# Performance work log

Measured on AMD Instinct MI355X. Metric: run time of the kernel, lower is better.

The kernel has to match this reference:

```python
import jax, jax.numpy as jnp
import numpy as np

N = 50000      # nodes
E = 800000     # edges
F = 64         # in_channels == out_channels
ED = 16        # edge_dim
G = 64         # graphs in batch
L = 2          # numLayers
BN_EPS = 1e-5
STD_EPS = 1e-5
AGG_DIM = F * 4 * 3  # 4 aggregators x 3 scalers


def setup_inputs() -> dict:
    key = jax.random.key(0)
    ks = jax.random.split(key, 12)
    r = lambda k, shp, fan: (jax.random.normal(k, shp, jnp.float32) / np.sqrt(fan)).astype(jnp.float32)
    return dict(
        x=jax.random.normal(ks[0], (N, F), jnp.float32),
        edge_attr=jax.random.normal(ks[1], (E, ED), jnp.float32),
        We=r(ks[2], (L, ED, F), ED), be=jnp.zeros((L, F), jnp.float32),
        Wpre=r(ks[3], (L, 3 * F, F), 3 * F), bpre=jnp.zeros((L, F), jnp.float32),
        Wpost=r(ks[4], (L, F + AGG_DIM, F), F + AGG_DIM), bpost=jnp.zeros((L, F), jnp.float32),
        Wlin=r(ks[5], (L, F, F), F), blin=jnp.zeros((L, F), jnp.float32),
        gamma=jnp.ones((L, F), jnp.float32), beta=jnp.zeros((L, F), jnp.float32),
        W1=r(ks[6], (F, 40), F), b1=jnp.zeros((40,), jnp.float32),
        W2=r(ks[7], (40, 1), 40), b2=jnp.zeros((1,), jnp.float32),
        edge_index=jax.random.randint(ks[8], (2, E), 0, N),
        batch=jnp.sort(jax.random.randint(ks[9], (N,), 0, G)),
    )


def _ceal_conv(x, src, dst, edge_attr, We, be, Wpre, bpre, Wpost, bpost, Wlin, blin, deg, amp, att):
    # PNA-style conv, towers=1, pre_layers=post_layers=1
    e = edge_attr @ We + be                                              # [E,F]
    h = jnp.concatenate([x[dst], x[src], e], axis=-1) @ Wpre + bpre      # [E,F]
    degc = jnp.maximum(deg, 1.0)[:, None]
    mean = jax.ops.segment_sum(h, dst, num_segments=N) / degc
    sq = jax.ops.segment_sum(h * h, dst, num_segments=N) / degc
    std = jnp.sqrt(jax.nn.relu(sq - mean * mean) + STD_EPS)
    has = (deg > 0)[:, None]
    mn = jnp.where(has, jax.ops.segment_min(h, dst, num_segments=N), 0.0)
    mx = jnp.where(has, jax.ops.segment_max(h, dst, num_segments=N), 0.0)
    aggs = jnp.concatenate([mean, mn, mx, std], axis=-1)                 # [N,4F]
    scaled = jnp.concatenate([aggs, aggs * amp[:, None], aggs * att[:, None]], axis=-1)  # [N,12F]
    out = jnp.concatenate([x, scaled], axis=-1) @ Wpost + bpost          # [N,F]
    return out @ Wlin + blin


def _bn(x, gamma, beta):
    mu = x.mean(0)
    var = x.var(0)  # biased, as torch BatchNorm training-mode normalization
    return (x - mu) * jax.lax.rsqrt(var + BN_EPS) * gamma + beta


def reference(x, edge_attr, We, be, Wpre, bpre, Wpost, bpost, Wlin, blin,
              gamma, beta, W1, b1, W2, b2, edge_index, batch):
    src, dst = edge_index[0], edge_index[1]
    deg = jax.ops.segment_sum(jnp.ones((E,), jnp.float32), dst, num_segments=N)
    avg_log = jnp.mean(jnp.log(deg + 1.0))
    logd = jnp.log(jnp.maximum(deg, 1.0) + 1.0)
    amp = logd / avg_log
    att = avg_log / logd
    for l in range(L):
        x = _ceal_conv(x, src, dst, edge_attr, We[l], be[l], Wpre[l], bpre[l],
                       Wpost[l], bpost[l], Wlin[l], blin[l], deg, amp, att)
        x = jax.nn.relu(_bn(x, gamma[l], beta[l]))
    cnt = jnp.maximum(jax.ops.segment_sum(jnp.ones((N,), jnp.float32), batch, num_segments=G), 1.0)
    gm = jax.ops.segment_sum(x, batch, num_segments=G) / cnt[:, None]    # global_mean_pool [G,F]
    return jax.nn.relu(gm @ W1 + b1) @ W2 + b2                           # [G,1]
```

## Files before the change

### kernel.cpp

```cpp
#include <hip/hip_runtime.h>
#include <math.h>
#include <float.h>

#define NN 50000
#define EE 800000
#define FF 64
#define EDIM 16
#define GG 64
#define NB64 782

typedef short bf16x8 __attribute__((ext_vector_type(8)));
typedef float f32x4 __attribute__((ext_vector_type(4)));

__device__ inline unsigned short bf_rne(float v) {
  unsigned int u = __float_as_uint(v);
  unsigned int r = (u + 0x7FFFu + ((u >> 16) & 1u)) >> 16;
  return (unsigned short)r;
}
__device__ inline float bf_up(unsigned short h) {
  return __uint_as_float(((unsigned int)h) << 16);
}
__device__ inline void split4(float4 v, ushort4& h, ushort4& l) {
  h.x = bf_rne(v.x); h.y = bf_rne(v.y); h.z = bf_rne(v.z); h.w = bf_rne(v.w);
  l.x = bf_rne(v.x - bf_up(h.x));
  l.y = bf_rne(v.y - bf_up(h.y));
  l.z = bf_rne(v.z - bf_up(h.z));
  l.w = bf_rne(v.w - bf_up(h.w));
}
__device__ inline float blo(unsigned int u) { return __uint_as_float(u << 16); }
__device__ inline float bhi(unsigned int u) { return __uint_as_float(u & 0xFFFF0000u); }

__global__ void k_deg(const int* __restrict__ eidx, int* __restrict__ deg) {
  int e = blockIdx.x * 256 + threadIdx.x;
  if (e < EE) atomicAdd(&deg[eidx[EE + e]], 1);
}

__global__ void k_avglog(const int* __restrict__ deg, double* __restrict__ acc) {
  int n = blockIdx.x * 256 + threadIdx.x;
  float v = (n < NN) ? logf((float)deg[n] + 1.0f) : 0.0f;
  __shared__ float s[256];
  s[threadIdx.x] = v;
  __syncthreads();
  for (int o = 128; o > 0; o >>= 1) {
    if (threadIdx.x < o) s[threadIdx.x] += s[threadIdx.x + o];
    __syncthreads();
  }
  if (threadIdx.x == 0) atomicAdd(acc, (double)s[0]);
}

__global__ __launch_bounds__(1024) void k_scan(const int* __restrict__ deg, int* __restrict__ offsets) {
  __shared__ int wsum[16];
  __shared__ int s_carry;
  int t = threadIdx.x;
  int lane = t & 63;
  int wid = t >> 6;
  if (t == 0) s_carry = 0;
  __syncthreads();
  for (int base = 0; base < NN; base += 1024) {
    int idx = base + t;
    int v = (idx < NN) ? deg[idx] : 0;
    int x = v;
    #pragma unroll
    for (int o = 1; o < 64; o <<= 1) {
      int y = __shfl_up(x, o);
      if (lane >= o) x += y;
    }
    if (lane == 63) wsum[wid] = x;
    __syncthreads();
    if (wid == 0 && lane < 16) {
      int wv = wsum[lane];
      #pragma unroll
      for (int o = 1; o < 16; o <<= 1) {
        int y = __shfl_up(wv, o);
        if (lane >= o) wv += y;
      }
      wsum[lane] = wv;
    }
    __syncthreads();
    int pre = (wid > 0 ? wsum[wid - 1] : 0) + s_carry;
    if (idx < NN) offsets[idx] = pre + x - v;
    __syncthreads();
    if (t == 0) s_carry += wsum[15];
    __syncthreads();
  }
  if (threadIdx.x == 0) offsets[NN] = s_carry;
}

__global__ void k_scatter(const int* __restrict__ eidx, const int* __restrict__ offsets,
                          int* __restrict__ cursor, int* __restrict__ srcs,
                          const float* __restrict__ eattr, unsigned int* __restrict__ PermEA) {
  int e = blockIdx.x * 256 + threadIdx.x;
  if (e < EE) {
    int s = eidx[e];
    int d = eidx[EE + e];
    int pos = offsets[d] + atomicAdd(&cursor[d], 1);
    srcs[pos] = s;
    const float4* ep = (const float4*)(eattr + (size_t)e * EDIM);
    float4 q0 = ep[0], q1 = ep[1], q2 = ep[2], q3 = ep[3];
    uint4 pa, pb;
    pa.x = (unsigned)bf_rne(q0.x) | ((unsigned)bf_rne(q0.y) << 16);
    pa.y = (unsigned)bf_rne(q0.z) | ((unsigned)bf_rne(q0.w) << 16);
    pa.z = (unsigned)bf_rne(q1.x) | ((unsigned)bf_rne(q1.y) << 16);
    pa.w = (unsigned)bf_rne(q1.z) | ((unsigned)bf_rne(q1.w) << 16);
    pb.x = (unsigned)bf_rne(q2.x) | ((unsigned)bf_rne(q2.y) << 16);
    pb.y = (unsigned)bf_rne(q2.z) | ((unsigned)bf_rne(q2.w) << 16);
    pb.z = (unsigned)bf_rne(q3.x) | ((unsigned)bf_rne(q3.y) << 16);
    pb.w = (unsigned)bf_rne(q3.z) | ((unsigned)bf_rne(q3.w) << 16);
    ((uint4*)PermEA)[(size_t)pos * 2] = pa;
    ((uint4*)PermEA)[(size_t)pos * 2 + 1] = pb;
  }
}

__global__ void k_ampatt(const int* __restrict__ deg, const double* __restrict__ acc,
                         float* __restrict__ amp, float* __restrict__ att) {
  int n = blockIdx.x * 256 + threadIdx.x;
  if (n < NN) {
    float avg = (float)(acc[0] / (double)NN);
    float d = (float)deg[n];
    float logd = logf(fmaxf(d, 1.0f) + 1.0f);
    amp[n] = logd / avg;
    att[n] = avg / logd;
  }
}

__global__ __launch_bounds__(256) void k_prep2(const float* __restrict__ We, const float* __restrict__ be,
                                               const float* __restrict__ Wpre, const float* __restrict__ bpre,
                                               const float* __restrict__ Wpost, const float* __restrict__ bpost,
                                               const float* __restrict__ Wlin, const float* __restrict__ blin,
                                               float* __restrict__ Mw, float* __restrict__ bconst,
                                               unsigned short* __restrict__ WcT_h, unsigned short* __restrict__ WcT_l,
                                               unsigned short* __restrict__ WxT_h, unsigned short* __restrict__ WxT_l,
                                               float* __restrict__ bcomb) {
  int id = blockIdx.x * 256 + threadIdx.x;
  if (id < 53248) {
    int k = id >> 6, f = id & 63;
    float a = 0.0f;
    for (int j = 0; j < FF; j++) a += Wpost[(size_t)k * FF + j] * Wlin[j * FF + f];
    unsigned short h = bf_rne(a);
    WcT_h[f * 832 + k] = h;
    WcT_l[f * 832 + k] = bf_rne(a - bf_up(h));
  } else if (id < 61440) {
    int lid = id - 53248;
    int j = lid >> 6, k = lid & 63;
    float v = (j < 64) ? Wpre[k * FF + j] : Wpre[(64 + k) * FF + (j - 64)];
    unsigned short h = bf_rne(v);
    WxT_h[j * 64 + k] = h;
    WxT_l[j * 64 + k] = bf_rne(v - bf_up(h));
  } else if (id < 62464) {
    int lid = id - 61440;
    int k = lid >> 6, f = lid & 63;
    float a = 0.0f;
    for (int j = 0; j < FF; j++) a += We[k * FF + j] * Wpre[(128 + j) * FF + f];
    Mw[k * FF + f] = a;
  } else {
    int f = threadIdx.x;
    if (blockIdx.x == 244 && f < 64) {
      float b = bpre[f];
      for (int j = 0; j < FF; j++) b += be[j] * Wpre[(128 + j) * FF + f];
      bconst[f] = b;
      float c = blin[f];
      for (int j = 0; j < FF; j++) c += bpost[j] * Wlin[j * FF + f];
      bcomb[f] = c;
    }
  }
}

__global__ __launch_bounds__(256) void k_xform(const float* __restrict__ x,
                                               const unsigned short* __restrict__ WxT_h,
                                               const unsigned short* __restrict__ WxT_l,
                                               float* __restrict__ Xd, float* __restrict__ Xs) {
  __shared__ unsigned short Ah[64 * 72], Al[64 * 72];
  __shared__ unsigned short Bh[128 * 72], Bl[128 * 72];
  int t = threadIdx.x;
  int n0 = blockIdx.x * 64;
  {
    int j = t >> 1, half = t & 1;
    const ushort4* srch = (const ushort4*)(WxT_h + j * 64 + half * 32);
    const ushort4* srcl = (const ushort4*)(WxT_l + j * 64 + half * 32);
    #pragma unroll
    for (int i = 0; i < 8; i++) {
      *(ushort4*)&Bh[j * 72 + half * 32 + i * 4] = srch[i];
      *(ushort4*)&Bl[j * 72 + half * 32 + i * 4] = srcl[i];
    }
  }
  {
    int r = t >> 2, c0 = (t & 3) * 16;
    int n = n0 + r;
    bool rok = n < NN;
    const float4* src = (const float4*)(x + (size_t)n * FF + c0);
    #pragma unroll
    for (int c4 = 0; c4 < 4; c4++) {
      float4 v = rok ? src[c4] : make_float4(0.f, 0.f, 0.f, 0.f);
      ushort4 h4, l4;
      split4(v, h4, l4);
      *(ushort4*)&Ah[r * 72 + c0 + c4 * 4] = h4;
      *(ushort4*)&Al[r * 72 + c0 + c4 * 4] = l4;
    }
  }
  __syncthreads();
  int lane = t & 63;
  int l15 = lane & 15;
  int quad = lane >> 4;
  int w = __builtin_amdgcn_readfirstlane(t >> 6);
  int rbase = (w & 1) * 32;
  int cbase = (w >> 1) * 64;
  f32x4 acc[2][4];
  #pragma unroll
  for (int rt = 0; rt < 2; rt++)
    #pragma unroll
    for (int ct = 0; ct < 4; ct++) acc[rt][ct] = (f32x4){0.f, 0.f, 0.f, 0.f};

  #pragma unroll
  for (int ks = 0; ks < 2; ks++) {
    bf16x8 a_h[2], a_l[2];
    #pragma unroll
    for (int rt = 0; rt < 2; rt++) {
      int row = rbase + rt * 16 + l15;
      a_h[rt] = *(const bf16x8*)&Ah[row * 72 + ks * 32 + quad * 8];
      a_l[rt] = *(const bf16x8*)&Al[row * 72 + ks * 32 + quad * 8];
    }
    #pragma unroll
    for (int ct = 0; ct < 4; ct++) {
      int col = cbase + ct * 16 + l15;
      bf16x8 b_h = *(const bf16x8*)&Bh[col * 72 + ks * 32 + quad * 8];
      bf16x8 b_l = *(const bf16x8*)&Bl[col * 72 + ks * 32 + quad * 8];
      #pragma unroll
      for (int rt = 0; rt < 2; rt++) {
        acc[rt][ct] = __builtin_amdgcn_mfma_f32_16x16x32_bf16(a_h[rt], b_h, acc[rt][ct], 0, 0, 0);
        acc[rt][ct] = __builtin_amdgcn_mfma_f32_16x16x32_bf16(a_h[rt], b_l, acc[rt][ct], 0, 0, 0);
        acc[rt][ct] = __builtin_amdgcn_mfma_f32_16x16x32_bf16(a_l[rt], b_h, acc[rt][ct], 0, 0, 0);
      }
    }
  }
  #pragma unroll
  for (int rt = 0; rt < 2; rt++) {
    #pragma unroll
    for (int ct = 0; ct < 4; ct++) {
      int col = cbase + ct * 16 + l15;
      float* dst = (col < 64) ? (Xd + col) : (Xs + col - 64);
      #pragma unroll
      for (int reg = 0; reg < 4; reg++) {
        int n = n0 + rbase + rt * 16 + quad * 4 + reg;
        if (n < NN) dst[(size_t)n * FF] = acc[rt][ct][reg];
      }
    }
  }
}

__global__ __launch_bounds__(256) void k_agg(const int* __restrict__ srcs, const int* __restrict__ offsets,
                                             const unsigned int* __restrict__ PermEA,
                                             const float* __restrict__ Mw, const float* __restrict__ bconst,
                                             const float* __restrict__ Xd, const float* __restrict__ Xs,
                                             float* __restrict__ aggs) {
  int wid = __builtin_amdgcn_readfirstlane(threadIdx.x >> 6);
  int lane = threadIdx.x & 63;
  int n = blockIdx.x * 4 + wid;
  if (n >= NN) return;
  float mw[16];
  #pragma unroll
  for (int k = 0; k < 16; k++) mw[k] = Mw[k * FF + lane];
  float base_h = Xd[(size_t)n * FF + lane] + bconst[lane];
  int o0 = offsets[n], o1 = offsets[n + 1];
  float s = 0.f, sq = 0.f, mn = FLT_MAX, mx = -FLT_MAX;

  for (int base = o0; base < o1; base += 64) {
    int m = min(64, o1 - base);
    int sv = 0;
    if (base + lane < o1) sv = srcs[base + lane];
    for (int j = 0; j < m; j++) {
      int src = __shfl(sv, j);
      float xs = Xs[(size_t)src * FF + lane];
      const uint4* q = (const uint4*)PermEA + (size_t)(base + j) * 2;
      uint4 qa = q[0], qb = q[1];
      float et = blo(qa.x) * mw[0]  + bhi(qa.x) * mw[1]
               + blo(qa.y) * mw[2]  + bhi(qa.y) * mw[3]
               + blo(qa.z) * mw[4]  + bhi(qa.z) * mw[5]
               + blo(qa.w) * mw[6]  + bhi(qa.w) * mw[7]
               + blo(qb.x) * mw[8]  + bhi(qb.x) * mw[9]
               + blo(qb.y) * mw[10] + bhi(qb.y) * mw[11]
               + blo(qb.z) * mw[12] + bhi(qb.z) * mw[13]
               + blo(qb.w) * mw[14] + bhi(qb.w) * mw[15];
      float h = base_h + xs + et;
      s += h;
      sq += h * h;
      mn = fminf(mn, h);
      mx = fmaxf(mx, h);
    }
  }
  float d = (float)(o1 - o0);
  float dc = fmaxf(d, 1.0f);
  float mean = s / dc;
  float msq = sq / dc;
  float sd = sqrtf(fmaxf(msq - mean * mean, 0.0f) + 1e-5f);
  bool has = d > 0.0f;
  float vmn = has ? mn : 0.0f;
  float vmx = has ? mx : 0.0f;
  size_t b = (size_t)n * 256;
  aggs[b + lane] = mean;
  aggs[b + 64 + lane] = vmn;
  aggs[b + 128 + lane] = vmx;
  aggs[b + 192 + lane] = sd;
}

__global__ __launch_bounds__(256) void k_post(const float* __restrict__ x, const float* __restrict__ aggs,
                                              const float* __restrict__ amp, const float* __restrict__ att,
                                              const unsigned short* __restrict__ WcT_h,
                                              const unsigned short* __restrict__ WcT_l,
                                              const float* __restrict__ bcomb,
                                              float* __restrict__ y, float* __restrict__ partials) {
  __shared__ unsigned short Ah[64 * 72], Al[64 * 72];
  __shared__ unsigned short Bh[64 * 72], Bl[64 * 72];
  __shared__ float red_s[4][32], red_q[4][32];
  int t = threadIdx.x;
  int n0 = blockIdx.x * 64;
  int lane = t & 63;
  int l15 = lane & 15;
  int quad = lane >> 4;
  int w = __builtin_amdgcn_readfirstlane(t >> 6);
  int rbase = (w & 1) * 32;
  int cbase = (w >> 1) * 32;

  int ar = t >> 2;
  int ac0 = (t & 3) * 16;
  int an = n0 + ar;
  bool rok = an < NN;
  float sc_amp = rok ? amp[an] : 0.f;
  float sc_att = rok ? att[an] : 0.f;
  const float* xrow = x + (size_t)an * FF;
  const float* arow = aggs + (size_t)an * 256;

  f32x4 acc[2][2];
  #pragma unroll
  for (int rt = 0; rt < 2; rt++)
    #pragma unroll
    for (int ct = 0; ct < 2; ct++) acc[rt][ct] = (f32x4){0.f, 0.f, 0.f, 0.f};

  for (int kc = 0; kc < 13; kc++) {
    const float* srcb;
    float scale = 1.0f;
    if (kc == 0) {
      srcb = xrow;
    } else {
      int kcm = kc - 1;
      srcb = arow + (kcm & 3) * 64;
      int sel = kcm >> 2;
      scale = (sel == 0) ? 1.0f : (sel == 1 ? sc_amp : sc_att);
    }
    #pragma unroll
    for (int c4 = 0; c4 < 4; c4++) {
      float4 v = rok ? *(const float4*)(srcb + ac0 + c4 * 4) : make_float4(0.f, 0.f, 0.f, 0.f);
      v.x *= scale; v.y *= scale; v.z *= scale; v.w *= scale;
      ushort4 h4, l4;
      split4(v, h4, l4);
      *(ushort4*)&Ah[ar * 72 + ac0 + c4 * 4] = h4;
      *(ushort4*)&Al[ar * 72 + ac0 + c4 * 4] = l4;
    }
    {
      int kbase = kc * 64;
      const ushort4* sh = (const ushort4*)(WcT_h + ar * 832 + kbase + ac0);
      const ushort4* sl = (const ushort4*)(WcT_l + ar * 832 + kbase + ac0);
      #pragma unroll
      for (int i = 0; i < 4; i++) {
        *(ushort4*)&Bh[ar * 72 + ac0 + i * 4] = sh[i];
        *(ushort4*)&Bl[ar * 72 + ac0 + i * 4] = sl[i];
      }
    }
    __syncthreads();
    #pragma unroll
    for (int ks = 0; ks < 2; ks++) {
      bf16x8 a_h[2], a_l[2], b_h[2], b_l[2];
      #pragma unroll
      for (int rt = 0; rt < 2; rt++) {
        int row = rbase + rt * 16 + l15;
        a_h[rt] = *(const bf16x8*)&Ah[row * 72 + ks * 32 + quad * 8];
        a_l[rt] = *(const bf16x8*)&Al[row * 72 + ks * 32 + quad * 8];
      }
      #pragma unroll
      for (int ct = 0; ct < 2; ct++) {
        int col = cbase + ct * 16 + l15;
        b_h[ct] = *(const bf16x8*)&Bh[col * 72 + ks * 32 + quad * 8];
        b_l[ct] = *(const bf16x8*)&Bl[col * 72 + ks * 32 + quad * 8];
      }
      #pragma unroll
      for (int rt = 0; rt < 2; rt++)
        #pragma unroll
        for (int ct = 0; ct < 2; ct++) {
          acc[rt][ct] = __builtin_amdgcn_mfma_f32_16x16x32_bf16(a_h[rt], b_h[ct], acc[rt][ct], 0, 0, 0);
          acc[rt][ct] = __builtin_amdgcn_mfma_f32_16x16x32_bf16(a_h[rt], b_l[ct], acc[rt][ct], 0, 0, 0);
          acc[rt][ct] = __builtin_amdgcn_mfma_f32_16x16x32_bf16(a_l[rt], b_h[ct], acc[rt][ct], 0, 0, 0);
        }
    }
    __syncthreads();
  }

  float ps[2] = {0.f, 0.f}, pq[2] = {0.f, 0.f};
  #pragma unroll
  for (int ct = 0; ct < 2; ct++) {
    int col = cbase + ct * 16 + l15;
    float bc = bcomb[col];
    #pragma unroll
    for (int rt = 0; rt < 2; rt++) {
      #pragma unroll
      for (int reg = 0; reg < 4; reg++) {
        int n = n0 + rbase + rt * 16 + quad * 4 + reg;
        float v = acc[rt][ct][reg] + bc;
        if (n < NN) {
          y[(size_t)n * FF + col] = v;
          ps[ct] += v;
          pq[ct] += v * v;
        }
      }
    }
  }
  #pragma unroll
  for (int ct = 0; ct < 2; ct++) {
    ps[ct] += __shfl_xor(ps[ct], 16);
    ps[ct] += __shfl_xor(ps[ct], 32);
    pq[ct] += __shfl_xor(pq[ct], 16);
    pq[ct] += __shfl_xor(pq[ct], 32);
  }
  if (quad == 0) {
    #pragma unroll
    for (int ct = 0; ct < 2; ct++) {
      red_s[w][ct * 16 + l15] = ps[ct];
      red_q[w][ct * 16 + l15] = pq[ct];
    }
  }
  __syncthreads();
  if (t < 64) {
    float ss, qq;
    if (t < 32) { ss = red_s[0][t] + red_s[1][t]; qq = red_q[0][t] + red_q[1][t]; }
    else        { ss = red_s[2][t - 32] + red_s[3][t - 32]; qq = red_q[2][t - 32] + red_q[3][t - 32]; }
    partials[(size_t)blockIdx.x * 128 + t] = ss;
    partials[(size_t)blockIdx.x * 128 + 64 + t] = qq;
  }
}

__global__ __launch_bounds__(1024) void k_bnfin(const float* __restrict__ partials,
                                                const float* __restrict__ gamma, const float* __restrict__ beta,
                                                float* __restrict__ scb) {
  __shared__ float red[1024];
  __shared__ double tot[128];
  int t = threadIdx.x;
  int c = t & 127, seg = t >> 7;
  float s = 0.f;
  for (int i = seg; i < NB64; i += 8) s += partials[(size_t)i * 128 + c];
  red[t] = s;
  __syncthreads();
  if (t < 128) {
    double d = 0.0;
    #pragma unroll
    for (int sg = 0; sg < 8; sg++) d += (double)red[sg * 128 + t];
    tot[t] = d;
  }
  __syncthreads();
  if (t < 64) {
    double mu = tot[t] / (double)NN;
    double var = tot[64 + t] / (double)NN - mu * mu;
    float sc = gamma[t] * rsqrtf((float)fmax(var, 0.0) + 1e-5f);
    scb[t] = sc;
    scb[64 + t] = beta[t] - (float)mu * sc;
  }
}

__global__ __launch_bounds__(256) void k_bnapply(const float* __restrict__ y, const float* __restrict__ scb,
                                                 float* __restrict__ xout) {
  int idx = blockIdx.x * 256 + threadIdx.x;
  if (idx >= NN * 16) return;
  int f4 = idx & 15;
  float4 v = ((const float4*)y)[idx];
  float4 sc = ((const float4*)scb)[f4];
  float4 of = ((const float4*)(scb + 64))[f4];
  v.x = fmaxf(v.x * sc.x + of.x, 0.0f);
  v.y = fmaxf(v.y * sc.y + of.y, 0.0f);
  v.z = fmaxf(v.z * sc.z + of.z, 0.0f);
  v.w = fmaxf(v.w * sc.w + of.w, 0.0f);
  ((float4*)xout)[idx] = v;
}

__global__ __launch_bounds__(256) void k_pool(const float* __restrict__ x, const int* __restrict__ batch,
                                              float* __restrict__ psum, float* __restrict__ cnt) {
  int lane = threadIdx.x & 63;
  int wv = threadIdx.x >> 6;
  int wglobal = blockIdx.x * 4 + wv;
  int nw = gridDim.x * 4;
  int per = (NN + nw - 1) / nw;
  int n0 = wglobal * per;
  int n1 = min(n0 + per, NN);
  if (n0 >= n1) return;
  int gcur = batch[n0];
  float acc = 0.0f;
  int count = 0;
  for (int n = n0; n < n1; n++) {
    int g = batch[n];
    float v = x[(size_t)n * FF + lane];
    if (g != gcur) {
      atomicAdd(&psum[gcur * FF + lane], acc);
      if (lane == 0) atomicAdd(&cnt[gcur], (float)count);
      gcur = g; acc = 0.0f; count = 0;
    }
    acc += v;
    count++;
  }
  atomicAdd(&psum[gcur * FF + lane], acc);
  if (lane == 0) atomicAdd(&cnt[gcur], (float)count);
}

__global__ void k_final(const float* __restrict__ psum, const float* __restrict__ cnt,
                        const float* __restrict__ W1, const float* __restrict__ b1,
                        const float* __restrict__ W2, const float* __restrict__ b2, float* __restrict__ out) {
  int g = threadIdx.x;
  if (g >= GG) return;
  float c = fmaxf(cnt[g], 1.0f);
  float gm[64];
  #pragma unroll
  for (int i = 0; i < 64; i++) gm[i] = psum[g * FF + i] / c;
  float o = b2[0];
  for (int h = 0; h < 40; h++) {
    float a = b1[h];
    #pragma unroll
    for (int i = 0; i < 64; i++) a += gm[i] * W1[i * 40 + h];
    o += fmaxf(a, 0.0f) * W2[h];
  }
  out[g] = o;
}

extern "C" void kernel_launch(void* const* d_in, const int* in_sizes, int n_in,
                              void* d_out, int out_size, void* d_ws, size_t ws_size,
                              hipStream_t stream) {
  (void)in_sizes; (void)n_in; (void)out_size; (void)ws_size;
  const float* x0    = (const float*)d_in[0];
  const float* eattr = (const float*)d_in[1];
  const float* We    = (const float*)d_in[2];
  const float* be    = (const float*)d_in[3];
  const float* Wpre  = (const float*)d_in[4];
  const float* bpre  = (const float*)d_in[5];
  const float* Wpost = (const float*)d_in[6];
  const float* bpost = (const float*)d_in[7];
  const float* Wlin  = (const float*)d_in[8];
  const float* blin  = (const float*)d_in[9];
  const float* gamma = (const float*)d_in[10];
  const float* beta  = (const float*)d_in[11];
  const float* W1    = (const float*)d_in[12];
  const float* b1    = (const float*)d_in[13];
  const float* W2    = (const float*)d_in[14];
  const float* b2    = (const float*)d_in[15];
  const int* eidx    = (const int*)d_in[16];
  const int* batch   = (const int*)d_in[17];
  float* out = (float*)d_out;

  char* w = (char*)d_ws;
  size_t off = 0;
  auto alloc = [&](size_t bytes) -> void* {
    void* p = w + off;
    off += bytes;
    off = (off + 255) & ~(size_t)255;
    return p;
  };
  int*    deg     = (int*)alloc(NN * sizeof(int));
  int*    offsets = (int*)alloc((NN + 1) * sizeof(int));
  int*    cursor  = (int*)alloc(NN * sizeof(int));
  int*    srcs    = (int*)alloc(EE * sizeof(int));
  unsigned int* PermEA = (unsigned int*)alloc((size_t)EE * 8 * sizeof(unsigned int));
  double* avgacc  = (double*)alloc(sizeof(double));
  float*  amp     = (float*)alloc(NN * sizeof(float));
  float*  att     = (float*)alloc(NN * sizeof(float));
  float*  Mw      = (float*)alloc(EDIM * FF * sizeof(float));
  float*  bconst  = (float*)alloc(FF * sizeof(float));
  float*  bcomb   = (float*)alloc(FF * sizeof(float));
  float*  scb     = (float*)alloc(2 * FF * sizeof(float));
  unsigned short* WcT_h = (unsigned short*)alloc(FF * 832 * sizeof(unsigned short));
  unsigned short* WcT_l = (unsigned short*)alloc(FF * 832 * sizeof(unsigned short));
  unsigned short* WxT_h = (unsigned short*)alloc(128 * 64 * sizeof(unsigned short));
  unsigned short* WxT_l = (unsigned short*)alloc(128 * 64 * sizeof(unsigned short));
  float*  partials = (float*)alloc((size_t)NB64 * 128 * sizeof(float));
  float*  Xd      = (float*)alloc((size_t)NN * FF * sizeof(float));
  float*  Xs      = (float*)alloc((size_t)NN * FF * sizeof(float));
  float*  aggs    = (float*)alloc((size_t)NN * 256 * sizeof(float));
  float*  ybuf    = (float*)alloc((size_t)NN * FF * sizeof(float));
  float*  psum    = (float*)alloc((GG * FF + GG) * sizeof(float));
  float*  cnt     = psum + GG * FF;

  hipMemsetAsync(deg, 0, NN * sizeof(int), stream);
  hipMemsetAsync(cursor, 0, NN * sizeof(int), stream);
  hipMemsetAsync(avgacc, 0, sizeof(double), stream);
  hipMemsetAsync(psum, 0, (GG * FF + GG) * sizeof(float), stream);

  k_deg<<<(EE + 255) / 256, 256, 0, stream>>>(eidx, deg);
  k_avglog<<<(NN + 255) / 256, 256, 0, stream>>>(deg, avgacc);
  k_scan<<<1, 1024, 0, stream>>>(deg, offsets);
  k_scatter<<<(EE + 255) / 256, 256, 0, stream>>>(eidx, offsets, cursor, srcs, eattr, PermEA);
  k_ampatt<<<(NN + 255) / 256, 256, 0, stream>>>(deg, avgacc, amp, att);

  const float* xin = x0;
  for (int l = 0; l < 2; l++) {
    k_prep2<<<245, 256, 0, stream>>>(We + l * EDIM * FF, be + l * FF, Wpre + (size_t)l * 3 * FF * FF,
                                     bpre + l * FF, Wpost + (size_t)l * 832 * FF, bpost + l * FF,
                                     Wlin + l * FF * FF, blin + l * FF,
                                     Mw, bconst, WcT_h, WcT_l, WxT_h, WxT_l, bcomb);
    k_xform<<<NB64, 256, 0, stream>>>(xin, WxT_h, WxT_l, Xd, Xs);
    k_agg<<<(NN + 3) / 4, 256, 0, stream>>>(srcs, offsets, PermEA, Mw, bconst, Xd, Xs, aggs);
    k_post<<<NB64, 256, 0, stream>>>(xin, aggs, amp, att, WcT_h, WcT_l, bcomb, ybuf, partials);
    k_bnfin<<<1, 1024, 0, stream>>>(partials, gamma + l * FF, beta + l * FF, scb);
    k_bnapply<<<(NN * 16 + 255) / 256, 256, 0, stream>>>(ybuf, scb, ybuf);
    xin = ybuf;
  }
  k_pool<<<200, 256, 0, stream>>>(ybuf, batch, psum, cnt);
  k_final<<<1, 64, 0, stream>>>(psum, cnt, W1, b1, W2, b2, out);
}
```

Before: 640.2 us.

## Fuse BatchNorm apply into consumers and parallelize degree prefix scan

After: 591.8 us. 7.6% less time.

```diff
diff --git a/kernel.cpp b/kernel.cpp
--- a/kernel.cpp
+++ b/kernel.cpp
@@ -8,6 +8,7 @@
 #define EDIM 16
 #define GG 64
 #define NB64 782
+#define NSB 196
 
 typedef short bf16x8 __attribute__((ext_vector_type(8)));
 typedef float f32x4 __attribute__((ext_vector_type(4)));
@@ -35,55 +36,78 @@
   if (e < EE) atomicAdd(&deg[eidx[EE + e]], 1);
 }
 
-__global__ void k_avglog(const int* __restrict__ deg, double* __restrict__ acc) {
-  int n = blockIdx.x * 256 + threadIdx.x;
-  float v = (n < NN) ? logf((float)deg[n] + 1.0f) : 0.0f;
-  __shared__ float s[256];
-  s[threadIdx.x] = v;
-  __syncthreads();
-  for (int o = 128; o > 0; o >>= 1) {
-    if (threadIdx.x < o) s[threadIdx.x] += s[threadIdx.x + o];
-    __syncthreads();
-  }
-  if (threadIdx.x == 0) atomicAdd(acc, (double)s[0]);
-}
-
-__global__ __launch_bounds__(1024) void k_scan(const int* __restrict__ deg, int* __restrict__ offsets) {
-  __shared__ int wsum[16];
-  __shared__ int s_carry;
+__global__ __launch_bounds__(256) void k_scanA(const int* __restrict__ deg, int* __restrict__ offsets,
+                                               int* __restrict__ bsum, float* __restrict__ lsum) {
+  __shared__ int ws[4];
+  __shared__ float lw[4];
   int t = threadIdx.x;
   int lane = t & 63;
-  int wid = t >> 6;
-  if (t == 0) s_carry = 0;
+  int wv = t >> 6;
+  int i = blockIdx.x * 256 + t;
+  int v = (i < NN) ? deg[i] : 0;
+  float lg = (i < NN) ? logf((float)v + 1.0f) : 0.0f;
+  int x = v;
+  #pragma unroll
+  for (int o = 1; o < 64; o <<= 1) {
+    int y = __shfl_up(x, o);
+    if (lane >= o) x += y;
+  }
+  #pragma unroll
+  for (int o = 1; o < 64; o <<= 1) lg += __shfl_xor(lg, o);
+  if (lane == 63) ws[wv] = x;
+  if (lane == 0) lw[wv] = lg;
   __syncthreads();
-  for (int base = 0; base < NN; base += 1024) {
-    int idx = base + t;
-    int v = (idx < NN) ? deg[idx] : 0;
-    int x = v;
-    #pragma unroll
-    for (int o = 1; o < 64; o <<= 1) {
-      int y = __shfl_up(x, o);
-      if (lane >= o) x += y;
-    }
-    if (lane == 63) wsum[wid] = x;
-    __syncthreads();
-    if (wid == 0 && lane < 16) {
-      int wv = wsum[lane];
-      #pragma unroll
-      for (int o = 1; o < 16; o <<= 1) {
-        int y = __shfl_up(wv, o);
-        if (lane >= o) wv += y;
-      }
-      wsum[lane] = wv;
-    }
-    __syncthreads();
-    int pre = (wid > 0 ? wsum[wid - 1] : 0) + s_carry;
-    if (idx < NN) offsets[idx] = pre + x - v;
-    __syncthreads();
-    if (t == 0) s_carry += wsum[15];
-    __syncthreads();
-  }
-  if (threadIdx.x == 0) offsets[NN] = s_carry;
+  int pre = 0;
+  for (int k = 0; k < wv; k++) pre += ws[k];
+  if (i < NN) offsets[i] = pre + x - v;
+  if (t == 0) {
+    bsum[blockIdx.x] = ws[0] + ws[1] + ws[2] + ws[3];
+    lsum[blockIdx.x] = lw[0] + lw[1] + lw[2] + lw[3];
+  }
+}
+
+__global__ __launch_bounds__(256) void k_scanB(const int* __restrict__ bsum, const float* __restrict__ lsum,
+                                               int* __restrict__ bpref, float* __restrict__ meta,
+                                               float* __restrict__ scbA) {
+  __shared__ int ws[4];
+  __shared__ float lw[4];
+  int t = threadIdx.x;
+  int lane = t & 63;
+  int wv = t >> 6;
+  int v = (t < NSB) ? bsum[t] : 0;
+  float lg = (t < NSB) ? lsum[t] : 0.0f;
+  int x = v;
+  #pragma unroll
+  for (int o = 1; o < 64; o <<= 1) {
+    int y = __shfl_up(x, o);
+    if (lane >= o) x += y;
+  }
+  #pragma unroll
+  for (int o = 1; o < 64; o <<= 1) lg += __shfl_xor(lg, o);
+  if (lane == 63) ws[wv] = x;
+  if (lane == 0) lw[wv] = lg;
+  __syncthreads();
+  int pre = 0;
+  for (int k = 0; k < wv; k++) pre += ws[k];
+  if (t < NSB) bpref[t] = pre + x - v;
+  if (t == 0) meta[0] = (lw[0] + lw[1] + lw[2] + lw[3]) / (float)NN;
+  if (t < 64) { scbA[t] = 1.0f; scbA[64 + t] = 0.0f; }
+  if (t == 0) scbA[128] = -FLT_MAX;
+}
+
+__global__ __launch_bounds__(256) void k_scanC(int* __restrict__ offsets, const int* __restrict__ bpref,
+                                               const int* __restrict__ deg, const float* __restrict__ meta,
+                                               float* __restrict__ amp, float* __restrict__ att) {
+  int i = blockIdx.x * 256 + threadIdx.x;
+  if (i < NN) {
+    offsets[i] += bpref[blockIdx.x];
+    float d = (float)deg[i];
+    float avg = meta[0];
+    float logd = logf(fmaxf(d, 1.0f) + 1.0f);
+    amp[i] = logd / avg;
+    att[i] = avg / logd;
+  }
+  if (i == 0) offsets[NN] = EE;
 }
 
 __global__ void k_scatter(const int* __restrict__ eidx, const int* __restrict__ offsets,
@@ -108,18 +132,6 @@
     pb.w = (unsigned)bf_rne(q3.z) | ((unsigned)bf_rne(q3.w) << 16);
     ((uint4*)PermEA)[(size_t)pos * 2] = pa;
     ((uint4*)PermEA)[(size_t)pos * 2 + 1] = pb;
-  }
-}
-
-__global__ void k_ampatt(const int* __restrict__ deg, const double* __restrict__ acc,
-                         float* __restrict__ amp, float* __restrict__ att) {
-  int n = blockIdx.x * 256 + threadIdx.x;
-  if (n < NN) {
-    float avg = (float)(acc[0] / (double)NN);
-    float d = (float)deg[n];
-    float logd = logf(fmaxf(d, 1.0f) + 1.0f);
-    amp[n] = logd / avg;
-    att[n] = avg / logd;
   }
 }
 
@@ -165,7 +177,7 @@
   }
 }
 
-__global__ __launch_bounds__(256) void k_xform(const float* __restrict__ x,
+__global__ __launch_bounds__(256) void k_xform(const float* __restrict__ x, const float* __restrict__ scb,
                                                const unsigned short* __restrict__ WxT_h,
                                                const unsigned short* __restrict__ WxT_l,
                                                float* __restrict__ Xd, float* __restrict__ Xs) {
@@ -188,9 +200,16 @@
     int n = n0 + r;
     bool rok = n < NN;
     const float4* src = (const float4*)(x + (size_t)n * FF + c0);
+    float flr = scb[128];
     #pragma unroll
     for (int c4 = 0; c4 < 4; c4++) {
       float4 v = rok ? src[c4] : make_float4(0.f, 0.f, 0.f, 0.f);
+      float4 sc = ((const float4*)scb)[(c0 >> 2) + c4];
+      float4 of = ((const float4*)(scb + 64))[(c0 >> 2) + c4];
+      v.x = fmaxf(v.x * sc.x + of.x, flr);
+      v.y = fmaxf(v.y * sc.y + of.y, flr);
+      v.z = fmaxf(v.z * sc.z + of.z, flr);
+      v.w = fmaxf(v.w * sc.w + of.w, flr);
       ushort4 h4, l4;
       split4(v, h4, l4);
       *(ushort4*)&Ah[r * 72 + c0 + c4 * 4] = h4;
@@ -302,7 +321,8 @@
   aggs[b + 192 + lane] = sd;
 }
 
-__global__ __launch_bounds__(256) void k_post(const float* __restrict__ x, const float* __restrict__ aggs,
+__global__ __launch_bounds__(256) void k_post(const float* __restrict__ x, const float* __restrict__ scb,
+                                              const float* __restrict__ aggs,
                                               const float* __restrict__ amp, const float* __restrict__ att,
                                               const unsigned short* __restrict__ WcT_h,
                                               const unsigned short* __restrict__ WcT_l,
@@ -328,6 +348,7 @@
   float sc_att = rok ? att[an] : 0.f;
   const float* xrow = x + (size_t)an * FF;
   const float* arow = aggs + (size_t)an * 256;
+  float flr = scb[128];
 
   f32x4 acc[2][2];
   #pragma unroll
@@ -336,24 +357,35 @@
     for (int ct = 0; ct < 2; ct++) acc[rt][ct] = (f32x4){0.f, 0.f, 0.f, 0.f};
 
   for (int kc = 0; kc < 13; kc++) {
-    const float* srcb;
-    float scale = 1.0f;
     if (kc == 0) {
-      srcb = xrow;
+      #pragma unroll
+      for (int c4 = 0; c4 < 4; c4++) {
+        float4 v = rok ? *(const float4*)(xrow + ac0 + c4 * 4) : make_float4(0.f, 0.f, 0.f, 0.f);
+        float4 sc = ((const float4*)scb)[(ac0 >> 2) + c4];
+        float4 of = ((const float4*)(scb + 64))[(ac0 >> 2) + c4];
+        v.x = fmaxf(v.x * sc.x + of.x, flr);
+        v.y = fmaxf(v.y * sc.y + of.y, flr);
+        v.z = fmaxf(v.z * sc.z + of.z, flr);
+        v.w = fmaxf(v.w * sc.w + of.w, flr);
+        ushort4 h4, l4;
+        split4(v, h4, l4);
+        *(ushort4*)&Ah[ar * 72 + ac0 + c4 * 4] = h4;
+        *(ushort4*)&Al[ar * 72 + ac0 + c4 * 4] = l4;
+      }
     } else {
       int kcm = kc - 1;
-      srcb = arow + (kcm & 3) * 64;
+      const float* srcb = arow + (kcm & 3) * 64;
       int sel = kcm >> 2;
-      scale = (sel == 0) ? 1.0f : (sel == 1 ? sc_amp : sc_att);
-    }
-    #pragma unroll
-    for (int c4 = 0; c4 < 4; c4++) {
-      float4 v = rok ? *(const float4*)(srcb + ac0 + c4 * 4) : make_float4(0.f, 0.f, 0.f, 0.f);
-      v.x *= scale; v.y *= scale; v.z *= scale; v.w *= scale;
-      ushort4 h4, l4;
-      split4(v, h4, l4);
-      *(ushort4*)&Ah[ar * 72 + ac0 + c4 * 4] = h4;
-      *(ushort4*)&Al[ar * 72 + ac0 + c4 * 4] = l4;
+      float scale = (sel == 0) ? 1.0f : (sel == 1 ? sc_amp : sc_att);
+      #pragma unroll
+      for (int c4 = 0; c4 < 4; c4++) {
+        float4 v = rok ? *(const float4*)(srcb + ac0 + c4 * 4) : make_float4(0.f, 0.f, 0.f, 0.f);
+        v.x *= scale; v.y *= scale; v.z *= scale; v.w *= scale;
+        ushort4 h4, l4;
+        split4(v, h4, l4);
+        *(ushort4*)&Ah[ar * 72 + ac0 + c4 * 4] = h4;
+        *(ushort4*)&Al[ar * 72 + ac0 + c4 * 4] = l4;
+      }
     }
     {
       int kbase = kc * 64;
@@ -461,24 +493,11 @@
     scb[t] = sc;
     scb[64 + t] = beta[t] - (float)mu * sc;
   }
-}
-
-__global__ __launch_bounds__(256) void k_bnapply(const float* __restrict__ y, const float* __restrict__ scb,
-                                                 float* __restrict__ xout) {
-  int idx = blockIdx.x * 256 + threadIdx.x;
-  if (idx >= NN * 16) return;
-  int f4 = idx & 15;
-  float4 v = ((const float4*)y)[idx];
-  float4 sc = ((const float4*)scb)[f4];
-  float4 of = ((const float4*)(scb + 64))[f4];
-  v.x = fmaxf(v.x * sc.x + of.x, 0.0f);
-  v.y = fmaxf(v.y * sc.y + of.y, 0.0f);
-  v.z = fmaxf(v.z * sc.z + of.z, 0.0f);
-  v.w = fmaxf(v.w * sc.w + of.w, 0.0f);
-  ((float4*)xout)[idx] = v;
-}
-
-__global__ __launch_bounds__(256) void k_pool(const float* __restrict__ x, const int* __restrict__ batch,
+  if (t == 0) scb[128] = 0.0f;
+}
+
+__global__ __launch_bounds__(256) void k_pool(const float* __restrict__ x, const float* __restrict__ scb,
+                                              const int* __restrict__ batch,
                                               float* __restrict__ psum, float* __restrict__ cnt) {
   int lane = threadIdx.x & 63;
   int wv = threadIdx.x >> 6;
@@ -488,12 +507,13 @@
   int n0 = wglobal * per;
   int n1 = min(n0 + per, NN);
   if (n0 >= n1) return;
+  float sc = scb[lane], of = scb[64 + lane], flr = scb[128];
   int gcur = batch[n0];
   float acc = 0.0f;
   int count = 0;
   for (int n = n0; n < n1; n++) {
     int g = batch[n];
-    float v = x[(size_t)n * FF + lane];
+    float v = fmaxf(x[(size_t)n * FF + lane] * sc + of, flr);
     if (g != gcur) {
       atomicAdd(&psum[gcur * FF + lane], acc);
       if (lane == 0) atomicAdd(&cnt[gcur], (float)count);
@@ -562,13 +582,17 @@
   int*    cursor  = (int*)alloc(NN * sizeof(int));
   int*    srcs    = (int*)alloc(EE * sizeof(int));
   unsigned int* PermEA = (unsigned int*)alloc((size_t)EE * 8 * sizeof(unsigned int));
-  double* avgacc  = (double*)alloc(sizeof(double));
+  int*    bsum    = (int*)alloc(NSB * sizeof(int));
+  int*    bpref   = (int*)alloc(NSB * sizeof(int));
+  float*  lsum    = (float*)alloc(NSB * sizeof(float));
+  float*  meta    = (float*)alloc(sizeof(float));
   float*  amp     = (float*)alloc(NN * sizeof(float));
   float*  att     = (float*)alloc(NN * sizeof(float));
   float*  Mw      = (float*)alloc(EDIM * FF * sizeof(float));
   float*  bconst  = (float*)alloc(FF * sizeof(float));
   float*  bcomb   = (float*)alloc(FF * sizeof(float));
-  float*  scb     = (float*)alloc(2 * FF * sizeof(float));
+  float*  scbA    = (float*)alloc(129 * sizeof(float));
+  float*  scbB    = (float*)alloc(2 * 129 * sizeof(float));
   unsigned short* WcT_h = (unsigned short*)alloc(FF * 832 * sizeof(unsigned short));
   unsigned short* WcT_l = (unsigned short*)alloc(FF * 832 * sizeof(unsigned short));
   unsigned short* WxT_h = (unsigned short*)alloc(128 * 64 * sizeof(unsigned short));
@@ -583,28 +607,28 @@
 
   hipMemsetAsync(deg, 0, NN * sizeof(int), stream);
   hipMemsetAsync(cursor, 0, NN * sizeof(int), stream);
-  hipMemsetAsync(avgacc, 0, sizeof(double), stream);
   hipMemsetAsync(psum, 0, (GG * FF + GG) * sizeof(float), stream);
 
   k_deg<<<(EE + 255) / 256, 256, 0, stream>>>(eidx, deg);
-  k_avglog<<<(NN + 255) / 256, 256, 0, stream>>>(deg, avgacc);
-  k_scan<<<1, 1024, 0, stream>>>(deg, offsets);
+  k_scanA<<<NSB, 256, 0, stream>>>(deg, offsets, bsum, lsum);
+  k_scanB<<<1, 256, 0, stream>>>(bsum, lsum, bpref, meta, scbA);
+  k_scanC<<<NSB, 256, 0, stream>>>(offsets, bpref, deg, meta, amp, att);
   k_scatter<<<(EE + 255) / 256, 256, 0, stream>>>(eidx, offsets, cursor, srcs, eattr, PermEA);
-  k_ampatt<<<(NN + 255) / 256, 256, 0, stream>>>(deg, avgacc, amp, att);
 
   const float* xin = x0;
+  const float* scb_in = scbA;
   for (int l = 0; l < 2; l++) {
     k_prep2<<<245, 256, 0, stream>>>(We + l * EDIM * FF, be + l * FF, Wpre + (size_t)l * 3 * FF * FF,
                                      bpre + l * FF, Wpost + (size_t)l * 832 * FF, bpost + l * FF,
                                      Wlin + l * FF * FF, blin + l * FF,
                                      Mw, bconst, WcT_h, WcT_l, WxT_h, WxT_l, bcomb);
-    k_xform<<<NB64, 256, 0, stream>>>(xin, WxT_h, WxT_l, Xd, Xs);
+    k_xform<<<NB64, 256, 0, stream>>>(xin, scb_in, WxT_h, WxT_l, Xd, Xs);
     k_agg<<<(NN + 3) / 4, 256, 0, stream>>>(srcs, offsets, PermEA, Mw, bconst, Xd, Xs, aggs);
-    k_post<<<NB64, 256, 0, stream>>>(xin, aggs, amp, att, WcT_h, WcT_l, bcomb, ybuf, partials);
-    k_bnfin<<<1, 1024, 0, stream>>>(partials, gamma + l * FF, beta + l * FF, scb);
-    k_bnapply<<<(NN * 16 + 255) / 256, 256, 0, stream>>>(ybuf, scb, ybuf);
+    k_post<<<NB64, 256, 0, stream>>>(xin, scb_in, aggs, amp, att, WcT_h, WcT_l, bcomb, ybuf, partials);
+    k_bnfin<<<1, 1024, 0, stream>>>(partials, gamma + l * FF, beta + l * FF, scbB + l * 129);
     xin = ybuf;
-  }
-  k_pool<<<200, 256, 0, stream>>>(ybuf, batch, psum, cnt);
+    scb_in = scbB + l * 129;
+  }
+  k_pool<<<200, 256, 0, stream>>>(ybuf, scbB + 129, batch, psum, cnt);
   k_final<<<1, 64, 0, stream>>>(psum, cnt, W1, b1, W2, b2, out);
 }
```
